# Optimization experiments

Measured on AMD Instinct MI355X. Metric: run time of the kernel, lower is better.

The kernel has to match this reference:

```python
import jax, jax.numpy as jnp
import numpy as np

S, B, IN, OUT = 32, 256, 1024, 1024

def setup_inputs() -> dict:
    key = jax.random.key(0)
    ks = jax.random.split(key, 7)
    return {
        "input": jax.random.normal(ks[0], (S, B, IN), dtype=jnp.float32),
        "weight_mu": jax.random.normal(ks[1], (OUT, IN), dtype=jnp.float32) * 0.1,
        "weight_rho": jax.random.normal(ks[2], (OUT, IN), dtype=jnp.float32) - 3.0,
        "bias_mu": jax.random.normal(ks[3], (OUT,), dtype=jnp.float32) * 0.1,
        "bias_rho": jax.random.normal(ks[4], (OUT,), dtype=jnp.float32) - 3.0,
        "eps_w": jax.random.normal(ks[5], (S, OUT, IN), dtype=jnp.float32),
        "eps_b": jax.random.normal(ks[6], (S, OUT), dtype=jnp.float32),
    }

def reference(input, weight_mu, weight_rho, bias_mu, bias_rho, eps_w, eps_b):
    # sigma = log(1 + exp(rho))  (softplus)
    weight_sigma = jax.nn.softplus(weight_rho)              # (out, in)
    bias_sigma = jax.nn.softplus(bias_rho)                  # (out,)
    # reparameterized samples: (S, out, in) and (S, out)
    weight = weight_mu[None, :, :] + weight_sigma[None, :, :] * eps_w
    bias = bias_mu[None, :] + bias_sigma[None, :] * eps_b
    # batch_linear: per-sample x @ W^T + b
    out = jnp.einsum('sbi,soi->sbo', input, weight) + bias[:, None, :]
    return out
```

## Files before the change

kernel.cpp:

```cpp
#include <hip/hip_runtime.h>
#include <hip/hip_bf16.h>

constexpr int kS   = 32;
constexpr int kB   = 256;
constexpr int kIN  = 1024;
constexpr int kOUT = 1024;
constexpr int BN   = 32;
constexpr int BK   = 32;
constexpr int LS   = 40;

typedef __bf16 v4bf __attribute__((ext_vector_type(4)));
typedef __bf16 v8bf __attribute__((ext_vector_type(8)));
typedef float  v4f  __attribute__((ext_vector_type(4)));

__device__ __forceinline__ float softplus_f(float x) {
    return fmaxf(x, 0.0f) + log1pf(expf(-fabsf(x)));
}
__device__ __forceinline__ unsigned int bfbits(float x) {
    __bf16 h = (__bf16)x;
    unsigned short u;
    __builtin_memcpy(&u, &h, 2);
    return (unsigned int)u;
}
__device__ __forceinline__ float asf(unsigned int u) {
    float f; __builtin_memcpy(&f, &u, 4); return f;
}

__global__ void sigma_pack(const float* __restrict__ mu, const float* __restrict__ rho,
                           uint4* __restrict__ ms) {
    int gid = blockIdx.x * blockDim.x + threadIdx.x;
    float4 m = reinterpret_cast<const float4*>(mu)[gid];
    float4 r = reinterpret_cast<const float4*>(rho)[gid];
    uint4 o;
    o.x = bfbits(m.x) | (bfbits(softplus_f(r.x)) << 16);
    o.y = bfbits(m.y) | (bfbits(softplus_f(r.y)) << 16);
    o.z = bfbits(m.z) | (bfbits(softplus_f(r.z)) << 16);
    o.w = bfbits(m.w) | (bfbits(softplus_f(r.w)) << 16);
    ms[gid] = o;
}

__global__ void xcast_kernel(const float* __restrict__ X, __bf16* __restrict__ Xb) {
    size_t i = ((size_t)blockIdx.x * blockDim.x + threadIdx.x) * 8;
    float4 a = *reinterpret_cast<const float4*>(X + i);
    float4 b = *reinterpret_cast<const float4*>(X + i + 4);
    v8bf r;
    r[0] = (__bf16)a.x; r[1] = (__bf16)a.y; r[2] = (__bf16)a.z; r[3] = (__bf16)a.w;
    r[4] = (__bf16)b.x; r[5] = (__bf16)b.y; r[6] = (__bf16)b.z; r[7] = (__bf16)b.w;
    *reinterpret_cast<v8bf*>(Xb + i) = r;
}

#define GLDS16(g, l) __builtin_amdgcn_global_load_lds(                      \
    (const __attribute__((address_space(1))) void*)(g),                     \
    (__attribute__((address_space(3))) void*)(l), 16, 0, 0)

template<bool XBF>
__global__ __launch_bounds__(256, 4) void dv_main(
        const void* __restrict__ Xv,
        const unsigned int* __restrict__ MS,
        const float* __restrict__ Ew,
        const float* __restrict__ Bmu,
        const float* __restrict__ Brho,
        const float* __restrict__ Eb,
        float* __restrict__ O)
{
    __shared__ __attribute__((aligned(16))) __bf16 Xs[2][kB * BK];
    __shared__ __attribute__((aligned(16))) __bf16 Ws[2][BN * LS];

    const int tid  = threadIdx.x;
    const int bb   = blockIdx.x;
    const int xcd  = bb & 7;
    const int jj   = bb >> 3;
    const int s    = (xcd << 2) | (jj >> 5);
    const int ot   = jj & 31;
    const int o_base = ot * BN;

    const int lane = tid & 63, wv = tid >> 6;
    const int lr = lane & 15, kg = lane >> 4;
    const int wrow = tid >> 3, wc = tid & 7;

    const float*        Eg  = Ew + ((size_t)s * kOUT + o_base) * kIN;
    const unsigned int* MSg = MS + (size_t)o_base * kIN;
    const __bf16* Xb = (const __bf16*)Xv + (size_t)s * kB * kIN;
    const float*  Xg = (const float*)Xv + (size_t)s * kB * kIN;

    v4f acc[4][2] = {};
    float4 er;
    uint4  pr;

    if constexpr (XBF) {
        #pragma unroll
        for (int q = 0; q < 4; ++q) {
            int row = wv * 64 + q * 16 + (lane >> 2);
            int qg  = ((lane & 3) - (row >> 2)) & 3;
            GLDS16(Xb + (size_t)row * kIN + qg * 8, &Xs[0][(wv * 64 + q * 16) * BK]);
        }
    }
    er = *reinterpret_cast<const float4*>(Eg + (size_t)wrow * kIN + wc * 4);
    pr = *reinterpret_cast<const uint4*>(MSg + (size_t)wrow * kIN + wc * 4);

    for (int kk = 0; kk < kIN; kk += BK) {
        const int p = (kk >> 5) & 1;

        {
            v4bf w;
            w[0] = (__bf16)fmaf(asf(pr.x & 0xffff0000u), er.x, asf(pr.x << 16));
            w[1] = (__bf16)fmaf(asf(pr.y & 0xffff0000u), er.y, asf(pr.y << 16));
            w[2] = (__bf16)fmaf(asf(pr.z & 0xffff0000u), er.z, asf(pr.z << 16));
            w[3] = (__bf16)fmaf(asf(pr.w & 0xffff0000u), er.w, asf(pr.w << 16));
            *reinterpret_cast<v4bf*>(&Ws[p][wrow * LS + wc * 4]) = w;
        }
        if constexpr (!XBF) {
            #pragma unroll
            for (int f0 = 0; f0 < 8; ++f0) {
                int f = f0 * 256 + tid;
                int row = f >> 3, c = f & 7;
                float4 v = *reinterpret_cast<const float4*>(Xg + (size_t)row * kIN + kk + c * 4);
                int q = c >> 1, h = c & 1;
                int ql = (q + (row >> 2)) & 3;
                v4bf w;
                w[0] = (__bf16)v.x; w[1] = (__bf16)v.y; w[2] = (__bf16)v.z; w[3] = (__bf16)v.w;
                *reinterpret_cast<v4bf*>(&Xs[p][row * BK + ql * 8 + h * 4]) = w;
            }
        }
        __syncthreads();

        const int kk2 = kk + BK;
        if (kk2 < kIN) {
            const int p2 = p ^ 1;
            if constexpr (XBF) {
                #pragma unroll
                for (int q = 0; q < 4; ++q) {
                    int row = wv * 64 + q * 16 + (lane >> 2);
                    int qg  = ((lane & 3) - (row >> 2)) & 3;
                    GLDS16(Xb + (size_t)row * kIN + kk2 + qg * 8,
                           &Xs[p2][(wv * 64 + q * 16) * BK]);
                }
            }
            er = *reinterpret_cast<const float4*>(Eg + (size_t)wrow * kIN + kk2 + wc * 4);
            pr = *reinterpret_cast<const uint4*>(MSg + (size_t)wrow * kIN + kk2 + wc * 4);
        }

        v8bf a[4], b[2];
        #pragma unroll
        for (int mf = 0; mf < 4; ++mf) {
            int row = wv * 64 + mf * 16 + lr;
            int ql  = (kg + (row >> 2)) & 3;
            a[mf] = *reinterpret_cast<const v8bf*>(&Xs[p][row * BK + ql * 8]);
        }
        #pragma unroll
        for (int nf = 0; nf < 2; ++nf)
            b[nf] = *reinterpret_cast<const v8bf*>(&Ws[p][(nf * 16 + lr) * LS + kg * 8]);
        #pragma unroll
        for (int mf = 0; mf < 4; ++mf) {
            #pragma unroll
            for (int nf = 0; nf < 2; ++nf)
                acc[mf][nf] = __builtin_amdgcn_mfma_f32_16x16x32_bf16(a[mf], b[nf], acc[mf][nf], 0, 0, 0);
        }
    }

    float bias[2];
    #pragma unroll
    for (int nf = 0; nf < 2; ++nf) {
        int o = o_base + nf * 16 + lr;
        bias[nf] = fmaf(softplus_f(Brho[o]), Eb[(size_t)s * kOUT + o], Bmu[o]);
    }
    #pragma unroll
    for (int mf = 0; mf < 4; ++mf) {
        #pragma unroll
        for (int rr = 0; rr < 4; ++rr) {
            int mrow = wv * 64 + mf * 16 + kg * 4 + rr;
            float* orow = O + ((size_t)s * kB + mrow) * kOUT + o_base;
            #pragma unroll
            for (int nf = 0; nf < 2; ++nf)
                orow[nf * 16 + lr] = acc[mf][nf][rr] + bias[nf];
        }
    }
}

extern "C" void kernel_launch(void* const* d_in, const int* in_sizes, int n_in,
                              void* d_out, int out_size, void* d_ws, size_t ws_size,
                              hipStream_t stream) {
    const float* input = (const float*)d_in[0];
    const float* w_mu  = (const float*)d_in[1];
    const float* w_rho = (const float*)d_in[2];
    const float* b_mu  = (const float*)d_in[3];
    const float* b_rho = (const float*)d_in[4];
    const float* eps_w = (const float*)d_in[5];
    const float* eps_b = (const float*)d_in[6];
    float* out = (float*)d_out;

    const size_t ms_bytes  = (size_t)kOUT * kIN * 4;
    const size_t xbf_bytes = (size_t)kS * kB * kIN * sizeof(__bf16);
    const bool use_xbf = ws_size >= ms_bytes + xbf_bytes;

    unsigned int* ms = (unsigned int*)d_ws;
    __bf16* xbf = (__bf16*)((char*)d_ws + ms_bytes);

    sigma_pack<<<dim3((kOUT * kIN) / (256 * 4)), 256, 0, stream>>>(w_mu, w_rho, (uint4*)ms);

    dim3 grid(kS * (kOUT / BN));
    if (use_xbf) {
        xcast_kernel<<<dim3((size_t)kS * kB * kIN / (256 * 8)), 256, 0, stream>>>(input, xbf);
        dv_main<true><<<grid, 256, 0, stream>>>(xbf, ms, eps_w, b_mu, b_rho, eps_b, out);
    } else {
        dv_main<false><<<grid, 256, 0, stream>>>(input, ms, eps_w, b_mu, b_rho, eps_b, out);
    }
}
```

Before: 295.4 us.

## Widen N tile to 64 and stage weights in 256-wide K chunks

```diff
diff --git a/kernel.cpp b/kernel.cpp
--- a/kernel.cpp
+++ b/kernel.cpp
@@ -5,9 +5,9 @@
 constexpr int kB   = 256;
 constexpr int kIN  = 1024;
 constexpr int kOUT = 1024;
-constexpr int BN   = 32;
+constexpr int BN   = 64;
 constexpr int BK   = 32;
-constexpr int LS   = 40;
+constexpr int CK   = 256;
 
 typedef __bf16 v4bf __attribute__((ext_vector_type(4)));
 typedef __bf16 v8bf __attribute__((ext_vector_type(8)));
@@ -54,7 +54,7 @@
     (__attribute__((address_space(3))) void*)(l), 16, 0, 0)
 
 template<bool XBF>
-__global__ __launch_bounds__(256, 4) void dv_main(
+__global__ __launch_bounds__(256) void dv_main(
         const void* __restrict__ Xv,
         const unsigned int* __restrict__ MS,
         const float* __restrict__ Ew,
@@ -64,28 +64,25 @@
         float* __restrict__ O)
 {
     __shared__ __attribute__((aligned(16))) __bf16 Xs[2][kB * BK];
-    __shared__ __attribute__((aligned(16))) __bf16 Ws[2][BN * LS];
+    __shared__ __attribute__((aligned(16))) __bf16 Wc[BN * CK];
 
     const int tid  = threadIdx.x;
     const int bb   = blockIdx.x;
     const int xcd  = bb & 7;
     const int jj   = bb >> 3;
-    const int s    = (xcd << 2) | (jj >> 5);
-    const int ot   = jj & 31;
+    const int s    = (xcd << 2) | (jj & 3);
+    const int ot   = jj >> 2;
     const int o_base = ot * BN;
 
     const int lane = tid & 63, wv = tid >> 6;
     const int lr = lane & 15, kg = lane >> 4;
-    const int wrow = tid >> 3, wc = tid & 7;
 
     const float*        Eg  = Ew + ((size_t)s * kOUT + o_base) * kIN;
     const unsigned int* MSg = MS + (size_t)o_base * kIN;
     const __bf16* Xb = (const __bf16*)Xv + (size_t)s * kB * kIN;
     const float*  Xg = (const float*)Xv + (size_t)s * kB * kIN;
 
-    v4f acc[4][2] = {};
-    float4 er;
-    uint4  pr;
+    v4f acc[4][4] = {};
 
     if constexpr (XBF) {
         #pragma unroll
@@ -95,72 +92,94 @@
             GLDS16(Xb + (size_t)row * kIN + qg * 8, &Xs[0][(wv * 64 + q * 16) * BK]);
         }
     }
-    er = *reinterpret_cast<const float4*>(Eg + (size_t)wrow * kIN + wc * 4);
-    pr = *reinterpret_cast<const uint4*>(MSg + (size_t)wrow * kIN + wc * 4);
-
-    for (int kk = 0; kk < kIN; kk += BK) {
-        const int p = (kk >> 5) & 1;
-
-        {
-            v4bf w;
-            w[0] = (__bf16)fmaf(asf(pr.x & 0xffff0000u), er.x, asf(pr.x << 16));
-            w[1] = (__bf16)fmaf(asf(pr.y & 0xffff0000u), er.y, asf(pr.y << 16));
-            w[2] = (__bf16)fmaf(asf(pr.z & 0xffff0000u), er.z, asf(pr.z << 16));
-            w[3] = (__bf16)fmaf(asf(pr.w & 0xffff0000u), er.w, asf(pr.w << 16));
-            *reinterpret_cast<v4bf*>(&Ws[p][wrow * LS + wc * 4]) = w;
-        }
-        if constexpr (!XBF) {
-            #pragma unroll
-            for (int f0 = 0; f0 < 8; ++f0) {
-                int f = f0 * 256 + tid;
-                int row = f >> 3, c = f & 7;
-                float4 v = *reinterpret_cast<const float4*>(Xg + (size_t)row * kIN + kk + c * 4);
-                int q = c >> 1, h = c & 1;
-                int ql = (q + (row >> 2)) & 3;
-                v4bf w;
-                w[0] = (__bf16)v.x; w[1] = (__bf16)v.y; w[2] = (__bf16)v.z; w[3] = (__bf16)v.w;
-                *reinterpret_cast<v4bf*>(&Xs[p][row * BK + ql * 8 + h * 4]) = w;
-            }
+
+    for (int c = 0; c < 4; ++c) {
+        const int ck = c * CK;
+
+        #pragma unroll 2
+        for (int j = 0; j < 8; ++j) {
+            int slot = j * 256 + tid;
+            int row  = slot >> 5;
+            int ch   = slot & 31;
+            const float*        ep = Eg  + (size_t)row * kIN + ck + ch * 8;
+            const unsigned int* mp = MSg + (size_t)row * kIN + ck + ch * 8;
+            float4 e0 = *reinterpret_cast<const float4*>(ep);
+            float4 e1 = *reinterpret_cast<const float4*>(ep + 4);
+            uint4  p0 = *reinterpret_cast<const uint4*>(mp);
+            uint4  p1 = *reinterpret_cast<const uint4*>(mp + 4);
+            v8bf w;
+            w[0] = (__bf16)fmaf(asf(p0.x & 0xffff0000u), e0.x, asf(p0.x << 16));
+            w[1] = (__bf16)fmaf(asf(p0.y & 0xffff0000u), e0.y, asf(p0.y << 16));
+            w[2] = (__bf16)fmaf(asf(p0.z & 0xffff0000u), e0.z, asf(p0.z << 16));
+            w[3] = (__bf16)fmaf(asf(p0.w & 0xffff0000u), e0.w, asf(p0.w << 16));
+            w[4] = (__bf16)fmaf(asf(p1.x & 0xffff0000u), e1.x, asf(p1.x << 16));
+            w[5] = (__bf16)fmaf(asf(p1.y & 0xffff0000u), e1.y, asf(p1.y << 16));
+            w[6] = (__bf16)fmaf(asf(p1.z & 0xffff0000u), e1.z, asf(p1.z << 16));
+            w[7] = (__bf16)fmaf(asf(p1.w & 0xffff0000u), e1.w, asf(p1.w << 16));
+            int pos = (ch + 2 * row) & 31;
+            *reinterpret_cast<v8bf*>(&Wc[row * CK + pos * 8]) = w;
         }
         __syncthreads();
 
-        const int kk2 = kk + BK;
-        if (kk2 < kIN) {
-            const int p2 = p ^ 1;
+        for (int t = 0; t < 8; ++t) {
+            const int kt = c * 8 + t;
+            const int p  = kt & 1;
+
             if constexpr (XBF) {
+                if (kt + 1 < 32) {
+                    const int kk2 = (kt + 1) * BK;
+                    #pragma unroll
+                    for (int q = 0; q < 4; ++q) {
+                        int row = wv * 64 + q * 16 + (lane >> 2);
+                        int qg  = ((lane & 3) - (row >> 2)) & 3;
+                        GLDS16(Xb + (size_t)row * kIN + kk2 + qg * 8,
+                               &Xs[p ^ 1][(wv * 64 + q * 16) * BK]);
+                    }
+                }
+            } else {
                 #pragma unroll
-                for (int q = 0; q < 4; ++q) {
-                    int row = wv * 64 + q * 16 + (lane >> 2);
-                    int qg  = ((lane & 3) - (row >> 2)) & 3;
-                    GLDS16(Xb + (size_t)row * kIN + kk2 + qg * 8,
-                           &Xs[p2][(wv * 64 + q * 16) * BK]);
+                for (int f0 = 0; f0 < 8; ++f0) {
+                    int f = f0 * 256 + tid;
+                    int row = f >> 3, cc = f & 7;
+                    float4 v = *reinterpret_cast<const float4*>(
+                        Xg + (size_t)row * kIN + kt * BK + cc * 4);
+                    int q = cc >> 1, h = cc & 1;
+                    int ql = (q + (row >> 2)) & 3;
+                    v4bf w;
+                    w[0] = (__bf16)v.x; w[1] = (__bf16)v.y;
+                    w[2] = (__bf16)v.z; w[3] = (__bf16)v.w;
+                    *reinterpret_cast<v4bf*>(&Xs[p][row * BK + ql * 8 + h * 4]) = w;
                 }
-            }
-            er = *reinterpret_cast<const float4*>(Eg + (size_t)wrow * kIN + kk2 + wc * 4);
-            pr = *reinterpret_cast<const uint4*>(MSg + (size_t)wrow * kIN + kk2 + wc * 4);
-        }
-
-        v8bf a[4], b[2];
-        #pragma unroll
-        for (int mf = 0; mf < 4; ++mf) {
-            int row = wv * 64 + mf * 16 + lr;
-            int ql  = (kg + (row >> 2)) & 3;
-            a[mf] = *reinterpret_cast<const v8bf*>(&Xs[p][row * BK + ql * 8]);
-        }
-        #pragma unroll
-        for (int nf = 0; nf < 2; ++nf)
-            b[nf] = *reinterpret_cast<const v8bf*>(&Ws[p][(nf * 16 + lr) * LS + kg * 8]);
-        #pragma unroll
-        for (int mf = 0; mf < 4; ++mf) {
-            #pragma unroll
-            for (int nf = 0; nf < 2; ++nf)
-                acc[mf][nf] = __builtin_amdgcn_mfma_f32_16x16x32_bf16(a[mf], b[nf], acc[mf][nf], 0, 0, 0);
-        }
-    }
-
-    float bias[2];
+                __syncthreads();
+            }
+
+            v8bf a[4], b[4];
+            #pragma unroll
+            for (int mf = 0; mf < 4; ++mf) {
+                int row = wv * 64 + mf * 16 + lr;
+                int ql  = (kg + (row >> 2)) & 3;
+                a[mf] = *reinterpret_cast<const v8bf*>(&Xs[p][row * BK + ql * 8]);
+            }
+            #pragma unroll
+            for (int nf = 0; nf < 4; ++nf) {
+                int r   = nf * 16 + lr;
+                int pos = ((t * 4 + kg) + 2 * r) & 31;
+                b[nf] = *reinterpret_cast<const v8bf*>(&Wc[r * CK + pos * 8]);
+            }
+            #pragma unroll
+            for (int mf = 0; mf < 4; ++mf) {
+                #pragma unroll
+                for (int nf = 0; nf < 4; ++nf)
+                    acc[mf][nf] = __builtin_amdgcn_mfma_f32_16x16x32_bf16(
+                        a[mf], b[nf], acc[mf][nf], 0, 0, 0);
+            }
+            __syncthreads();
+        }
+    }
+
+    float bias[4];
     #pragma unroll
-    for (int nf = 0; nf < 2; ++nf) {
+    for (int nf = 0; nf < 4; ++nf) {
         int o = o_base + nf * 16 + lr;
         bias[nf] = fmaf(softplus_f(Brho[o]), Eb[(size_t)s * kOUT + o], Bmu[o]);
     }
@@ -171,7 +190,7 @@
             int mrow = wv * 64 + mf * 16 + kg * 4 + rr;
             float* orow = O + ((size_t)s * kB + mrow) * kOUT + o_base;
             #pragma unroll
-            for (int nf = 0; nf < 2; ++nf)
+            for (int nf = 0; nf < 4; ++nf)
                 orow[nf * 16 + lr] = acc[mf][nf][rr] + bias[nf];
         }
     }
```

New measurement: 260.9 us. 11.7% less time.
